# Optimization experiments

Measured on AMD Instinct MI355X. Metric: run time of the kernel, lower is better.

## Reference

```python
import jax, jax.numpy as jnp
import numpy as np

B, T, C = 512, 256, 384  # batch, seq (<= block_size 256), n_embed
HEAD = 64


def setup_inputs() -> dict:
    key = jax.random.key(0)
    k1, k2, k3, k4 = jax.random.split(key, 4)
    scale = 1.0 / np.sqrt(C)
    return {
        "x": jax.random.normal(k1, (B, T, C), dtype=jnp.float32),
        "Wq": jax.random.normal(k2, (C, HEAD), dtype=jnp.float32) * scale,
        "Wk": jax.random.normal(k3, (C, HEAD), dtype=jnp.float32) * scale,
        "Wv": jax.random.normal(k4, (C, HEAD), dtype=jnp.float32) * scale,
    }


def reference(x, Wq, Wk, Wv):
    # Single causal self-attention head (dropout in eval mode / identity).
    _, T_, C_ = x.shape
    q = x @ Wq  # [B,T,H]
    k = x @ Wk  # [B,T,H]
    v = x @ Wv  # [B,T,H]
    # NOTE: original scales by n_embed**-0.5 (C), not head_size**-0.5.
    wei = jnp.einsum('bth,bsh->bts', q, k) * (C_ ** -0.5)  # [B,T,T]
    causal = jnp.tril(jnp.ones((T_, T_), dtype=bool))
    wei = jnp.where(causal, wei, -jnp.inf)
    wei = jax.nn.softmax(wei, axis=-1)
    return jnp.einsum('bts,bsh->bth', wei, v)  # [B,T,H]
```

## Files before the change

kernel.cpp:

```cpp
#include <hip/hip_runtime.h>

#define B_ 512
#define T_ 256
#define C_ 384
#define H_ 64

typedef __attribute__((ext_vector_type(8))) short bf16x8;
typedef __attribute__((ext_vector_type(4))) float f32x4;

__device__ __forceinline__ short f2bf(float f) {
    unsigned u = __float_as_uint(f);
    u += 0x7fffu + ((u >> 16) & 1u);
    return (short)(u >> 16);
}

__device__ __forceinline__ bf16x8 cvt8(const float* p) {
    const float4* p4 = (const float4*)p;
    float4 a = p4[0], b = p4[1];
    bf16x8 r;
    r[0] = f2bf(a.x); r[1] = f2bf(a.y); r[2] = f2bf(a.z); r[3] = f2bf(a.w);
    r[4] = f2bf(b.x); r[5] = f2bf(b.y); r[6] = f2bf(b.z); r[7] = f2bf(b.w);
    return r;
}

__global__ void pack_w_kernel(const float* __restrict__ Wq, const float* __restrict__ Wk,
                              const float* __restrict__ Wv, short* __restrict__ wp) {
    int p = blockIdx.x * 256 + threadIdx.x;
    if (p >= 12 * 12 * 512) return;
    int j    = p & 7;
    int lane = (p >> 3) & 63;
    int pc   = p >> 9;
    int ct = pc % 12, ks = pc / 12;
    int n  = ct * 16 + (lane & 15);
    int kk = ks * 32 + (lane >> 4) * 8 + j;
    const float* src = (n < 64) ? Wq : ((n < 128) ? Wk : Wv);
    wp[p] = f2bf(src[kk * 64 + (n & 63)]);
}

__global__ __launch_bounds__(512, 2) void fused_kernel(
    const float* __restrict__ x, const short* __restrict__ wp,
    float* __restrict__ out) {
    __shared__ short Ks[32 * 512];
    __shared__ short Vs[32 * 512];
    __shared__ short Pb[8][16 * 40];

    const int b = blockIdx.x;
    const int tid = threadIdx.x;
    const int w = tid >> 6, lane = tid & 63;
    const int cl = lane & 15, quad = lane >> 4;

    const float* xb = x + (long)b * (T_ * C_);
    const int r0 = 16 * w;
    const int r1 = 240 - 16 * w;
    const float* xr0 = xb + (long)(r0 + cl) * C_;
    const float* xr1 = xb + (long)(r1 + cl) * C_;

    f32x4 acc[2][12];
    #pragma unroll
    for (int rt = 0; rt < 2; rt++)
        #pragma unroll
        for (int ct = 0; ct < 12; ct++) {
            f32x4 z = {0.f, 0.f, 0.f, 0.f};
            acc[rt][ct] = z;
        }

    const short* wl = wp + lane * 8;
    for (int ks = 0; ks < 12; ks++) {
        const int koff = ks * 32 + quad * 8;
        bf16x8 a0 = cvt8(xr0 + koff);
        bf16x8 a1 = cvt8(xr1 + koff);
        const short* wk = wl + ks * 6144;
        #pragma unroll
        for (int ct = 0; ct < 12; ct++) {
            bf16x8 bf = *(const bf16x8*)(wk + ct * 512);
            acc[0][ct] = __builtin_amdgcn_mfma_f32_16x16x32_bf16(a0, bf, acc[0][ct], 0, 0, 0);
            acc[1][ct] = __builtin_amdgcn_mfma_f32_16x16x32_bf16(a1, bf, acc[1][ct], 0, 0, 0);
        }
    }

    #pragma unroll
    for (int rt = 0; rt < 2; rt++) {
        const int tb = (rt ? r1 : r0) + quad * 4;
        #pragma unroll
        for (int ct = 4; ct < 8; ct++) {
            const int h = (ct - 4) * 16 + cl;
            const int kk = h >> 5, hq = (h & 31) >> 3, j = h & 7;
            #pragma unroll
            for (int r = 0; r < 4; r++) {
                const int t = tb + r;
                Ks[((t >> 4) * 2 + kk) * 512 + ((t & 15) + 16 * hq) * 8 + j] =
                    f2bf(acc[rt][ct][r]);
            }
        }
        #pragma unroll
        for (int ct = 8; ct < 12; ct++) {
            const int ht = ct - 8;
            #pragma unroll
            for (int r = 0; r < 4; r++) {
                const int t = tb + r;
                Vs[((t >> 5) * 4 + ht) * 512 + (cl + 16 * ((t >> 3) & 3)) * 8 + (t & 7)] =
                    f2bf(acc[rt][ct][r]);
            }
        }
    }

    short* pb = Pb[w];
    bf16x8 qf[2][2];
    #pragma unroll
    for (int rt = 0; rt < 2; rt++)
        #pragma unroll
        for (int kk = 0; kk < 2; kk++) {
            #pragma unroll
            for (int cth = 0; cth < 2; cth++) {
                const int ct = kk * 2 + cth;
                #pragma unroll
                for (int r = 0; r < 4; r++)
                    pb[(quad * 4 + r) * 40 + cth * 16 + cl] = f2bf(acc[rt][ct][r]);
            }
            __builtin_amdgcn_wave_barrier();
            qf[rt][kk] = *(const bf16x8*)(pb + cl * 40 + quad * 8);
            __builtin_amdgcn_wave_barrier();
        }

    __syncthreads();

    const float scale = 0.05103103630798287f;

    #pragma unroll
    for (int it = 0; it < 2; it++) {
        const int rg = it ? (15 - w) : w;
        const int base = rg << 4;
        const bf16x8 qf0 = qf[it][0];
        const bf16x8 qf1 = qf[it][1];

        f32x4 sacc[16];
        #pragma unroll
        for (int st = 0; st < 16; st++) {
            if (st > rg) continue;
            bf16x8 k0 = *(const bf16x8*)(Ks + (st * 2 + 0) * 512 + lane * 8);
            bf16x8 k1 = *(const bf16x8*)(Ks + (st * 2 + 1) * 512 + lane * 8);
            f32x4 z = {0.f, 0.f, 0.f, 0.f};
            f32x4 t = __builtin_amdgcn_mfma_f32_16x16x32_bf16(qf0, k0, z, 0, 0, 0);
            t = __builtin_amdgcn_mfma_f32_16x16x32_bf16(qf1, k1, t, 0, 0, 0);
            sacc[st] = t;
        }

        float m4[4] = {-3e38f, -3e38f, -3e38f, -3e38f};
        #pragma unroll
        for (int st = 0; st < 16; st++) {
            if (st > rg) continue;
            #pragma unroll
            for (int r = 0; r < 4; r++) {
                float sv = sacc[st][r] * scale;
                if (st * 16 + cl > base + quad * 4 + r) sv = -1e30f;
                sacc[st][r] = sv;
                m4[r] = fmaxf(m4[r], sv);
            }
        }
        #pragma unroll
        for (int d = 1; d < 16; d <<= 1)
            #pragma unroll
            for (int r = 0; r < 4; r++)
                m4[r] = fmaxf(m4[r], __shfl_xor(m4[r], d));

        float l4[4] = {0.f, 0.f, 0.f, 0.f};
        #pragma unroll
        for (int st = 0; st < 16; st++) {
            if (st > rg) continue;
            #pragma unroll
            for (int r = 0; r < 4; r++) {
                float pv = exp2f((sacc[st][r] - m4[r]) * 1.4426950408889634f);
                sacc[st][r] = pv;
                l4[r] += pv;
            }
        }
        #pragma unroll
        for (int d = 1; d < 16; d <<= 1)
            #pragma unroll
            for (int r = 0; r < 4; r++)
                l4[r] += __shfl_xor(l4[r], d);

        f32x4 oacc[4];
        #pragma unroll
        for (int ht = 0; ht < 4; ht++) {
            f32x4 z = {0.f, 0.f, 0.f, 0.f};
            oacc[ht] = z;
        }
        #pragma unroll
        for (int c = 0; c < 8; c++) {
            if (c > (rg >> 1)) continue;
            #pragma unroll
            for (int half = 0; half < 2; half++) {
                const int st = c * 2 + half;
                #pragma unroll
                for (int r = 0; r < 4; r++) {
                    short pv = (st <= rg) ? f2bf(sacc[st][r]) : (short)0;
                    pb[(quad * 4 + r) * 40 + half * 16 + cl] = pv;
                }
            }
            __builtin_amdgcn_wave_barrier();
            const bf16x8 pa = *(const bf16x8*)(pb + cl * 40 + quad * 8);
            #pragma unroll
            for (int ht = 0; ht < 4; ht++) {
                const bf16x8 vf = *(const bf16x8*)(Vs + (c * 4 + ht) * 512 + lane * 8);
                oacc[ht] = __builtin_amdgcn_mfma_f32_16x16x32_bf16(pa, vf, oacc[ht], 0, 0, 0);
            }
            __builtin_amdgcn_wave_barrier();
        }

        #pragma unroll
        for (int r = 0; r < 4; r++) {
            const float inv = 1.0f / l4[r];
            float* op = out + (long)(b * T_ + base + quad * 4 + r) * H_ + cl;
            #pragma unroll
            for (int ht = 0; ht < 4; ht++)
                op[ht * 16] = oacc[ht][r] * inv;
        }
    }
}

extern "C" void kernel_launch(void* const* d_in, const int* in_sizes, int n_in,
                              void* d_out, int out_size, void* d_ws, size_t ws_size,
                              hipStream_t stream) {
    const float* x  = (const float*)d_in[0];
    const float* Wq = (const float*)d_in[1];
    const float* Wk = (const float*)d_in[2];
    const float* Wv = (const float*)d_in[3];
    float* out = (float*)d_out;

    short* wp = (short*)d_ws;

    pack_w_kernel<<<288, 256, 0, stream>>>(Wq, Wk, Wv, wp);
    fused_kernel<<<B_, 512, 0, stream>>>(x, wp, out);
}
```

Before: 325.5 us.

## Use 16 waves per batch, one row tile each, with prefetched x loads

The block grows from 8 to 16 waves, so each wave projects and attends one 16-row tile instead of two paired tiles. Tiles are assigned through a swizzled mapping so that the causal work per SIMD stays balanced. The x loads are software-pipelined two k-steps ahead, and the softmax scale is folded into the log2e constant. This raises parallelism and latency hiding and halves accumulator registers per wave, at the cost of tighter register limits from launch_bounds(1024,4) and more threads contending in one block.

```diff
diff --git a/kernel.cpp b/kernel.cpp
--- a/kernel.cpp
+++ b/kernel.cpp
@@ -14,9 +14,7 @@
     return (short)(u >> 16);
 }
 
-__device__ __forceinline__ bf16x8 cvt8(const float* p) {
-    const float4* p4 = (const float4*)p;
-    float4 a = p4[0], b = p4[1];
+__device__ __forceinline__ bf16x8 pack8(float4 a, float4 b) {
     bf16x8 r;
     r[0] = f2bf(a.x); r[1] = f2bf(a.y); r[2] = f2bf(a.z); r[3] = f2bf(a.w);
     r[4] = f2bf(b.x); r[5] = f2bf(b.y); r[6] = f2bf(b.z); r[7] = f2bf(b.w);
@@ -37,185 +35,178 @@
     wp[p] = f2bf(src[kk * 64 + (n & 63)]);
 }
 
-__global__ __launch_bounds__(512, 2) void fused_kernel(
+__global__ __launch_bounds__(1024, 4) void fused_kernel(
     const float* __restrict__ x, const short* __restrict__ wp,
     float* __restrict__ out) {
     __shared__ short Ks[32 * 512];
     __shared__ short Vs[32 * 512];
-    __shared__ short Pb[8][16 * 40];
+    __shared__ short Pb[16][16 * 40];
 
     const int b = blockIdx.x;
     const int tid = threadIdx.x;
     const int w = tid >> 6, lane = tid & 63;
     const int cl = lane & 15, quad = lane >> 4;
 
+    const int rg = (w & 12) | ((w & 3) ^ (w >> 2));
+    const int base = rg << 4;
+
     const float* xb = x + (long)b * (T_ * C_);
-    const int r0 = 16 * w;
-    const int r1 = 240 - 16 * w;
-    const float* xr0 = xb + (long)(r0 + cl) * C_;
-    const float* xr1 = xb + (long)(r1 + cl) * C_;
-
-    f32x4 acc[2][12];
-    #pragma unroll
-    for (int rt = 0; rt < 2; rt++)
-        #pragma unroll
-        for (int ct = 0; ct < 12; ct++) {
-            f32x4 z = {0.f, 0.f, 0.f, 0.f};
-            acc[rt][ct] = z;
-        }
-
+    const float4* xr = (const float4*)(xb + (long)(base + cl) * C_) + quad * 2;
+
+    f32x4 acc[12];
+    #pragma unroll
+    for (int ct = 0; ct < 12; ct++) {
+        f32x4 z = {0.f, 0.f, 0.f, 0.f};
+        acc[ct] = z;
+    }
+
+    float4 xa[3][2];
+    xa[0][0] = xr[0]; xa[0][1] = xr[1];
+    xa[1][0] = xr[8]; xa[1][1] = xr[9];
     const short* wl = wp + lane * 8;
+    #pragma unroll
     for (int ks = 0; ks < 12; ks++) {
-        const int koff = ks * 32 + quad * 8;
-        bf16x8 a0 = cvt8(xr0 + koff);
-        bf16x8 a1 = cvt8(xr1 + koff);
+        if (ks < 10) {
+            xa[(ks + 2) % 3][0] = xr[(ks + 2) * 8];
+            xa[(ks + 2) % 3][1] = xr[(ks + 2) * 8 + 1];
+        }
+        bf16x8 a = pack8(xa[ks % 3][0], xa[ks % 3][1]);
         const short* wk = wl + ks * 6144;
         #pragma unroll
         for (int ct = 0; ct < 12; ct++) {
             bf16x8 bf = *(const bf16x8*)(wk + ct * 512);
-            acc[0][ct] = __builtin_amdgcn_mfma_f32_16x16x32_bf16(a0, bf, acc[0][ct], 0, 0, 0);
-            acc[1][ct] = __builtin_amdgcn_mfma_f32_16x16x32_bf16(a1, bf, acc[1][ct], 0, 0, 0);
-        }
-    }
-
-    #pragma unroll
-    for (int rt = 0; rt < 2; rt++) {
-        const int tb = (rt ? r1 : r0) + quad * 4;
-        #pragma unroll
-        for (int ct = 4; ct < 8; ct++) {
-            const int h = (ct - 4) * 16 + cl;
-            const int kk = h >> 5, hq = (h & 31) >> 3, j = h & 7;
+            acc[ct] = __builtin_amdgcn_mfma_f32_16x16x32_bf16(a, bf, acc[ct], 0, 0, 0);
+        }
+    }
+
+    const int tb = base + quad * 4;
+    #pragma unroll
+    for (int ct = 4; ct < 8; ct++) {
+        const int h = (ct - 4) * 16 + cl;
+        const int kk = h >> 5, hq = (h & 31) >> 3, j = h & 7;
+        #pragma unroll
+        for (int r = 0; r < 4; r++) {
+            const int t = tb + r;
+            Ks[((t >> 4) * 2 + kk) * 512 + ((t & 15) + 16 * hq) * 8 + j] =
+                f2bf(acc[ct][r]);
+        }
+    }
+    #pragma unroll
+    for (int ct = 8; ct < 12; ct++) {
+        const int ht = ct - 8;
+        #pragma unroll
+        for (int r = 0; r < 4; r++) {
+            const int t = tb + r;
+            Vs[((t >> 5) * 4 + ht) * 512 + (cl + 16 * ((t >> 3) & 3)) * 8 + (t & 7)] =
+                f2bf(acc[ct][r]);
+        }
+    }
+
+    short* pb = Pb[w];
+    bf16x8 qf[2];
+    #pragma unroll
+    for (int kk = 0; kk < 2; kk++) {
+        #pragma unroll
+        for (int cth = 0; cth < 2; cth++) {
+            const int ct = kk * 2 + cth;
+            #pragma unroll
+            for (int r = 0; r < 4; r++)
+                pb[(quad * 4 + r) * 40 + cth * 16 + cl] = f2bf(acc[ct][r]);
+        }
+        __builtin_amdgcn_wave_barrier();
+        qf[kk] = *(const bf16x8*)(pb + cl * 40 + quad * 8);
+        __builtin_amdgcn_wave_barrier();
+    }
+
+    __syncthreads();
+
+    const float scale2 = 0.05103103630798287f * 1.4426950408889634f;
+
+    const bf16x8 qf0 = qf[0];
+    const bf16x8 qf1 = qf[1];
+
+    f32x4 sacc[16];
+    #pragma unroll
+    for (int st = 0; st < 16; st++) {
+        if (st > rg) continue;
+        bf16x8 k0 = *(const bf16x8*)(Ks + (st * 2 + 0) * 512 + lane * 8);
+        bf16x8 k1 = *(const bf16x8*)(Ks + (st * 2 + 1) * 512 + lane * 8);
+        f32x4 z = {0.f, 0.f, 0.f, 0.f};
+        f32x4 t = __builtin_amdgcn_mfma_f32_16x16x32_bf16(qf0, k0, z, 0, 0, 0);
+        t = __builtin_amdgcn_mfma_f32_16x16x32_bf16(qf1, k1, t, 0, 0, 0);
+        sacc[st] = t;
+    }
+
+    float m4[4] = {-3e38f, -3e38f, -3e38f, -3e38f};
+    #pragma unroll
+    for (int st = 0; st < 16; st++) {
+        if (st > rg) continue;
+        #pragma unroll
+        for (int r = 0; r < 4; r++) {
+            float sv = sacc[st][r] * scale2;
+            if (st * 16 + cl > base + quad * 4 + r) sv = -1e30f;
+            sacc[st][r] = sv;
+            m4[r] = fmaxf(m4[r], sv);
+        }
+    }
+    #pragma unroll
+    for (int d = 1; d < 16; d <<= 1)
+        #pragma unroll
+        for (int r = 0; r < 4; r++)
+            m4[r] = fmaxf(m4[r], __shfl_xor(m4[r], d));
+
+    float l4[4] = {0.f, 0.f, 0.f, 0.f};
+    #pragma unroll
+    for (int st = 0; st < 16; st++) {
+        if (st > rg) continue;
+        #pragma unroll
+        for (int r = 0; r < 4; r++) {
+            float pv = exp2f(sacc[st][r] - m4[r]);
+            sacc[st][r] = pv;
+            l4[r] += pv;
+        }
+    }
+    #pragma unroll
+    for (int d = 1; d < 16; d <<= 1)
+        #pragma unroll
+        for (int r = 0; r < 4; r++)
+            l4[r] += __shfl_xor(l4[r], d);
+
+    f32x4 oacc[4];
+    #pragma unroll
+    for (int ht = 0; ht < 4; ht++) {
+        f32x4 z = {0.f, 0.f, 0.f, 0.f};
+        oacc[ht] = z;
+    }
+    #pragma unroll
+    for (int c = 0; c < 8; c++) {
+        if (c > (rg >> 1)) continue;
+        #pragma unroll
+        for (int half = 0; half < 2; half++) {
+            const int st = c * 2 + half;
             #pragma unroll
             for (int r = 0; r < 4; r++) {
-                const int t = tb + r;
-                Ks[((t >> 4) * 2 + kk) * 512 + ((t & 15) + 16 * hq) * 8 + j] =
-                    f2bf(acc[rt][ct][r]);
+                short pv = (st <= rg) ? f2bf(sacc[st][r]) : (short)0;
+                pb[(quad * 4 + r) * 40 + half * 16 + cl] = pv;
             }
         }
-        #pragma unroll
-        for (int ct = 8; ct < 12; ct++) {
-            const int ht = ct - 8;
-            #pragma unroll
-            for (int r = 0; r < 4; r++) {
-                const int t = tb + r;
-                Vs[((t >> 5) * 4 + ht) * 512 + (cl + 16 * ((t >> 3) & 3)) * 8 + (t & 7)] =
-                    f2bf(acc[rt][ct][r]);
-            }
-        }
-    }
-
-    short* pb = Pb[w];
-    bf16x8 qf[2][2];
-    #pragma unroll
-    for (int rt = 0; rt < 2; rt++)
-        #pragma unroll
-        for (int kk = 0; kk < 2; kk++) {
-            #pragma unroll
-            for (int cth = 0; cth < 2; cth++) {
-                const int ct = kk * 2 + cth;
-                #pragma unroll
-                for (int r = 0; r < 4; r++)
-                    pb[(quad * 4 + r) * 40 + cth * 16 + cl] = f2bf(acc[rt][ct][r]);
-            }
-            __builtin_amdgcn_wave_barrier();
-            qf[rt][kk] = *(const bf16x8*)(pb + cl * 40 + quad * 8);
-            __builtin_amdgcn_wave_barrier();
-        }
-
-    __syncthreads();
-
-    const float scale = 0.05103103630798287f;
-
-    #pragma unroll
-    for (int it = 0; it < 2; it++) {
-        const int rg = it ? (15 - w) : w;
-        const int base = rg << 4;
-        const bf16x8 qf0 = qf[it][0];
-        const bf16x8 qf1 = qf[it][1];
-
-        f32x4 sacc[16];
-        #pragma unroll
-        for (int st = 0; st < 16; st++) {
-            if (st > rg) continue;
-            bf16x8 k0 = *(const bf16x8*)(Ks + (st * 2 + 0) * 512 + lane * 8);
-            bf16x8 k1 = *(const bf16x8*)(Ks + (st * 2 + 1) * 512 + lane * 8);
-            f32x4 z = {0.f, 0.f, 0.f, 0.f};
-            f32x4 t = __builtin_amdgcn_mfma_f32_16x16x32_bf16(qf0, k0, z, 0, 0, 0);
-            t = __builtin_amdgcn_mfma_f32_16x16x32_bf16(qf1, k1, t, 0, 0, 0);
-            sacc[st] = t;
-        }
-
-        float m4[4] = {-3e38f, -3e38f, -3e38f, -3e38f};
-        #pragma unroll
-        for (int st = 0; st < 16; st++) {
-            if (st > rg) continue;
-            #pragma unroll
-            for (int r = 0; r < 4; r++) {
-                float sv = sacc[st][r] * scale;
-                if (st * 16 + cl > base + quad * 4 + r) sv = -1e30f;
-                sacc[st][r] = sv;
-                m4[r] = fmaxf(m4[r], sv);
-            }
-        }
-        #pragma unroll
-        for (int d = 1; d < 16; d <<= 1)
-            #pragma unroll
-            for (int r = 0; r < 4; r++)
-                m4[r] = fmaxf(m4[r], __shfl_xor(m4[r], d));
-
-        float l4[4] = {0.f, 0.f, 0.f, 0.f};
-        #pragma unroll
-        for (int st = 0; st < 16; st++) {
-            if (st > rg) continue;
-            #pragma unroll
-            for (int r = 0; r < 4; r++) {
-                float pv = exp2f((sacc[st][r] - m4[r]) * 1.4426950408889634f);
-                sacc[st][r] = pv;
-                l4[r] += pv;
-            }
-        }
-        #pragma unroll
-        for (int d = 1; d < 16; d <<= 1)
-            #pragma unroll
-            for (int r = 0; r < 4; r++)
-                l4[r] += __shfl_xor(l4[r], d);
-
-        f32x4 oacc[4];
+        __builtin_amdgcn_wave_barrier();
+        const bf16x8 pa = *(const bf16x8*)(pb + cl * 40 + quad * 8);
         #pragma unroll
         for (int ht = 0; ht < 4; ht++) {
-            f32x4 z = {0.f, 0.f, 0.f, 0.f};
-            oacc[ht] = z;
-        }
-        #pragma unroll
-        for (int c = 0; c < 8; c++) {
-            if (c > (rg >> 1)) continue;
-            #pragma unroll
-            for (int half = 0; half < 2; half++) {
-                const int st = c * 2 + half;
-                #pragma unroll
-                for (int r = 0; r < 4; r++) {
-                    short pv = (st <= rg) ? f2bf(sacc[st][r]) : (short)0;
-                    pb[(quad * 4 + r) * 40 + half * 16 + cl] = pv;
-                }
-            }
-            __builtin_amdgcn_wave_barrier();
-            const bf16x8 pa = *(const bf16x8*)(pb + cl * 40 + quad * 8);
-            #pragma unroll
-            for (int ht = 0; ht < 4; ht++) {
-                const bf16x8 vf = *(const bf16x8*)(Vs + (c * 4 + ht) * 512 + lane * 8);
-                oacc[ht] = __builtin_amdgcn_mfma_f32_16x16x32_bf16(pa, vf, oacc[ht], 0, 0, 0);
-            }
-            __builtin_amdgcn_wave_barrier();
-        }
-
-        #pragma unroll
-        for (int r = 0; r < 4; r++) {
-            const float inv = 1.0f / l4[r];
-            float* op = out + (long)(b * T_ + base + quad * 4 + r) * H_ + cl;
-            #pragma unroll
-            for (int ht = 0; ht < 4; ht++)
-                op[ht * 16] = oacc[ht][r] * inv;
-        }
+            const bf16x8 vf = *(const bf16x8*)(Vs + (c * 4 + ht) * 512 + lane * 8);
+            oacc[ht] = __builtin_amdgcn_mfma_f32_16x16x32_bf16(pa, vf, oacc[ht], 0, 0, 0);
+        }
+        __builtin_amdgcn_wave_barrier();
+    }
+
+    #pragma unroll
+    for (int r = 0; r < 4; r++) {
+        const float inv = 1.0f / l4[r];
+        float* op = out + (long)(b * T_ + base + quad * 4 + r) * H_ + cl;
+        #pragma unroll
+        for (int ht = 0; ht < 4; ht++)
+            op[ht * 16] = oacc[ht][r] * inv;
     }
 }
 
@@ -231,5 +222,5 @@
     short* wp = (short*)d_ws;
 
     pack_w_kernel<<<288, 256, 0, stream>>>(Wq, Wk, Wv, wp);
-    fused_kernel<<<B_, 512, 0, stream>>>(x, wp, out);
-}
+    fused_kernel<<<B_, 1024, 0, stream>>>(x, wp, out);
+}
```

New measurement: 331.5 us. Within noise of the previous version (+1.8%).
